# Performance work log

Hardware: AMD Instinct MI355X
Metric: run time of the kernel (lower is better)

## Reference

```python
import jax, jax.numpy as jnp
import numpy as np

B, S, D, H = 2, 2048, 1024, 16
HD = D // H  # 64
MASK_VAL = -10000.0


def setup_inputs() -> dict:
    key = jax.random.key(0)
    ks = jax.random.split(key, 8)
    sc = 0.02
    q_features = jax.random.normal(ks[0], (B, S, D), jnp.float32)
    kv_features = jax.random.normal(ks[1], (B, S, D), jnp.float32)
    # causal mask, broadcastable (1,1,S,S)
    mask = jnp.tril(jnp.ones((S, S), jnp.bool_))[None, None]
    Wq = jax.random.normal(ks[2], (D, D), jnp.float32) * sc
    bq = jnp.zeros((D,), jnp.float32)
    Wkv = jax.random.normal(ks[3], (D, 2 * D), jnp.float32) * sc
    bkv = jnp.zeros((2 * D,), jnp.float32)
    Wp = jax.random.normal(ks[4], (D, D), jnp.float32) * sc
    bp = jnp.zeros((D,), jnp.float32)
    return {"q_features": q_features, "kv_features": kv_features, "mask": mask,
            "Wq": Wq, "bq": bq, "Wkv": Wkv, "bkv": bkv, "Wp": Wp, "bp": bp}


def _split_heads(t):
    # (B,S,D) -> (B,H,S,HD)
    return t.reshape(B, S, H, HD).transpose(0, 2, 1, 3)


def reference(q_features, kv_features, mask, Wq, bq, Wkv, bkv, Wp, bp):
    query = q_features @ Wq + bq            # (B,S,D)
    kv = kv_features @ Wkv + bkv            # (B,S,2D)
    key, value = jnp.split(kv, 2, axis=-1)
    q = _split_heads(query)                 # (B,H,S,HD)
    k = _split_heads(key)
    v = _split_heads(value)
    scores = jnp.einsum('bhqd,bhkd->bhqk', q, k) / jnp.sqrt(jnp.float32(HD))
    scores = jnp.where(mask, scores, jnp.asarray(MASK_VAL, scores.dtype))
    attn = jax.nn.softmax(scores, axis=-1)  # (B,H,S,S)
    out = jnp.einsum('bhqk,bhkd->bhqd', attn, v)
    out = out.transpose(0, 2, 1, 3).reshape(B, S, D)  # merge heads
    return out @ Wp + bp
```

## Files before the change

### kernel.cpp

```cpp
#include <hip/hip_runtime.h>

typedef unsigned short u16;
typedef unsigned int u32;
typedef __attribute__((ext_vector_type(4))) unsigned short us4;
typedef __attribute__((ext_vector_type(8))) unsigned short us8;
typedef __attribute__((ext_vector_type(4))) short s16x4;
typedef __attribute__((ext_vector_type(8))) __bf16 bf16x8;
typedef __attribute__((ext_vector_type(4))) float floatx4;

#define S_ 2048
#define D_ 1024
#define QSC 0.18033688f

__device__ __forceinline__ float b2f(u16 u) {
  unsigned v = ((unsigned)u) << 16;
  return __builtin_bit_cast(float, v);
}
__device__ __forceinline__ u16 f2bf(float f) {
  unsigned u = __builtin_bit_cast(unsigned, f);
  unsigned r = (u + 0x7fffu + ((u >> 16) & 1u)) >> 16;
  return (u16)r;
}
__device__ __forceinline__ u16 f2bf_rhu(float f) {
  return (u16)((__builtin_bit_cast(unsigned, f) + 0x8000u) >> 16);
}

typedef const __attribute__((address_space(1))) u32* gas_t;
typedef __attribute__((address_space(3))) u32* las_t;
__device__ __forceinline__ void gload16(const u16* g, u16* l) {
  __builtin_amdgcn_global_load_lds((gas_t)g, (las_t)l, 16, 0, 0);
}

#define PBAR()                                   \
  {                                              \
    __builtin_amdgcn_sched_barrier(0);           \
    asm volatile("" ::: "memory");               \
    __builtin_amdgcn_s_barrier();                \
    asm volatile("" ::: "memory");               \
    __builtin_amdgcn_sched_barrier(0);           \
  }
#define WAITVM(N) asm volatile("s_waitcnt vmcnt(" #N ")" ::: "memory")

__global__ __launch_bounds__(256) void prep(
    const float* __restrict__ qf, const float* __restrict__ kvf,
    const float* __restrict__ Wq, const float* __restrict__ Wkv,
    const float* __restrict__ Wp, u16* __restrict__ qa, u16* __restrict__ kva,
    u16* __restrict__ Wqt, u16* __restrict__ Wkvt, u16* __restrict__ Wpt) {
  int bid = blockIdx.x, tid = threadIdx.x;
  if (bid < 4096) {
    const float* src = (bid < 2048) ? qf : kvf;
    u16* dst = (bid < 2048) ? qa : kva;
    size_t i = ((size_t)(bid & 2047) * 256 + tid) * 8;
    floatx4 a = *(const floatx4*)(src + i);
    floatx4 b = *(const floatx4*)(src + i + 4);
    us8 r;
#pragma unroll
    for (int j = 0; j < 4; j++) { r[j] = f2bf(a[j]); r[4 + j] = f2bf(b[j]); }
    *(us8*)(dst + i) = r;
  } else {
    int t = bid - 4096;
    const float* src; u16* dst; int R, C;
    if (t < 1024)      { src = Wq;  dst = Wqt;  R = 1024; C = 1024; }
    else if (t < 3072) { t -= 1024; src = Wkv; dst = Wkvt; R = 1024; C = 2048; }
    else               { t -= 3072; src = Wp;  dst = Wpt;  R = 1024; C = 1024; }
    int bx = t % (C >> 5), by = t / (C >> 5);
    __shared__ u16 tile[32][33];
    int tx = tid & 31, ty = tid >> 5;
    int x = bx * 32 + tx;
    for (int i = ty; i < 32; i += 8)
      tile[i][tx] = f2bf(src[(size_t)(by * 32 + i) * C + x]);
    __syncthreads();
    int r = tid >> 3, c4 = tid & 7;
    us4 v;
#pragma unroll
    for (int j = 0; j < 4; j++) v[j] = tile[c4 * 4 + j][r];
    *(us4*)&dst[(size_t)(bx * 32 + r) * R + by * 32 + c4 * 4] = v;
  }
}

template <int TM, int TN, int MODE>
__device__ __forceinline__ void gemm4w(
    const u16* __restrict__ A, const u16* __restrict__ Bt,
    const float* __restrict__ bias, void* __restrict__ C0,
    u16* __restrict__ C1, int N, int m0, int n0, u16* smem, float cscale) {
  constexpr int MF = TM / 32, NF = TN / 32;
  constexpr int ASZ = TM * 64;
  constexpr int SLOT = (TM + TN) * 64;
  int tid = threadIdx.x;
  int w = tid >> 6, lane = tid & 63;
  int quad = lane >> 4, l16 = lane & 15;
  int wr = w >> 1, wc = w & 1;

  int gch = ((lane & 7) ^ ((lane >> 3) & 7)) << 3;
  const u16* Ag = A + (size_t)(m0 + w * (TM / 4) + (lane >> 3)) * 1024 + gch;
  const u16* Bg = Bt + (size_t)(n0 + w * (TN / 4) + (lane >> 3)) * 1024 + gch;
  u16* Adst = smem + w * (TM / 4) * 64;
  u16* Bdst = smem + ASZ + w * (TN / 4) * 64;

  int ab = (wr * (TM / 2) + l16) * 64;
  int bb = ASZ + (wc * (TN / 2) + l16) * 64;
  int xk0 = (quad ^ (l16 & 7)) << 3;
  int xk1 = ((4 + quad) ^ (l16 & 7)) << 3;

  floatx4 acc[MF][NF] = {};

#define STAGE4(tn, s_)                                                  \
  {                                                                     \
    _Pragma("unroll") for (int i = 0; i < MF; i++)                      \
      gload16(Ag + (size_t)(tn) * 64 + (size_t)i * 8192,                \
              Adst + (s_) * SLOT + i * 512);                            \
    _Pragma("unroll") for (int i = 0; i < NF; i++)                      \
      gload16(Bg + (size_t)(tn) * 64 + (size_t)i * 8192,                \
              Bdst + (s_) * SLOT + i * 512);                            \
  }

#define COMPUTE4(SOFF)                                                  \
  {                                                                     \
    _Pragma("unroll") for (int kk = 0; kk < 2; kk++) {                  \
      int xk = kk ? xk1 : xk0;                                          \
      bf16x8 bfr[NF];                                                   \
      _Pragma("unroll") for (int nf = 0; nf < NF; nf++)                 \
        bfr[nf] = __builtin_bit_cast(bf16x8,                            \
            *(const us8*)&smem[(SOFF) + bb + nf * 1024 + xk]);          \
      _Pragma("unroll") for (int mf = 0; mf < MF; mf++) {               \
        bf16x8 afr = __builtin_bit_cast(bf16x8,                         \
            *(const us8*)&smem[(SOFF) + ab + mf * 1024 + xk]);          \
        _Pragma("unroll") for (int nf = 0; nf < NF; nf++)               \
          acc[mf][nf] = __builtin_amdgcn_mfma_f32_16x16x32_bf16(        \
              afr, bfr[nf], acc[mf][nf], 0, 0, 0);                      \
      }                                                                 \
    }                                                                   \
  }

  STAGE4(0, 0);
  WAITVM(0);
  PBAR();
#pragma unroll 1
  for (int t = 0; t < 16; t += 2) {
    STAGE4(t + 1, 1);
    COMPUTE4(0);
    WAITVM(0);
    PBAR();
    if (t + 2 < 16) STAGE4(t + 2, 0);
    COMPUTE4(SLOT);
    WAITVM(0);
    PBAR();
  }

#undef STAGE4
#undef COMPUTE4

#pragma unroll
  for (int mf = 0; mf < MF; mf++) {
#pragma unroll
    for (int nf = 0; nf < NF; nf++) {
      int col = n0 + wc * (TN / 2) + nf * 16 + l16;
      int rowq = m0 + wr * (TM / 2) + mf * 16 + quad * 4;
      float bv = bias[col];
      if (MODE == 0) {
        u16* o = (u16*)C0;
#pragma unroll
        for (int r = 0; r < 4; r++)
          o[(size_t)(rowq + r) * N + col] = f2bf((acc[mf][nf][r] + bv) * cscale);
      } else if (MODE == 1) {
        float* o = (float*)C0;
#pragma unroll
        for (int r = 0; r < 4; r++)
          o[(size_t)(rowq + r) * N + col] = acc[mf][nf][r] + bv;
      } else {
        if (col < 1024) {
          u16* o = (u16*)C0;
#pragma unroll
          for (int r = 0; r < 4; r++)
            o[(size_t)(rowq + r) * 1024 + col] = f2bf(acc[mf][nf][r] + bv);
        } else {
          int vcol = col - 1024;
          int b = rowq >> 11, s0 = rowq & 2047;
          us4 pv;
#pragma unroll
          for (int r = 0; r < 4; r++) pv[r] = f2bf(acc[mf][nf][r] + bv);
          *(us4*)&C1[((size_t)(b * 1024 + vcol)) * (size_t)S_ + s0] = pv;
        }
      }
    }
  }
}

__global__ __launch_bounds__(256, 2) void gemm_qkv(
    const u16* __restrict__ qa, const u16* __restrict__ kva,
    const u16* __restrict__ Wqt, const u16* __restrict__ Wkvt,
    const float* __restrict__ bq, const float* __restrict__ bkv,
    u16* __restrict__ Qb, u16* __restrict__ Kb, u16* __restrict__ Vt) {
  __shared__ __align__(16) u16 smem[32768];
  int bid = blockIdx.x;
  int work = (bid & 7) * 96 + (bid >> 3);
  if (work < 256) {
    gemm4w<128, 128, 0>(qa, Wqt, bq, Qb, nullptr, 1024,
                        (work >> 3) * 128, (work & 7) * 128, smem, QSC);
  } else {
    int lb = work - 256;
    gemm4w<128, 128, 2>(kva, Wkvt, bkv, Kb, Vt, 2048,
                        (lb >> 4) * 128, (lb & 15) * 128, smem, 1.0f);
  }
}

__global__ __launch_bounds__(256, 3) void gemm_out(
    const u16* __restrict__ AO, const u16* __restrict__ Wpt,
    const float* __restrict__ bp, float* __restrict__ out) {
  __shared__ __align__(16) u16 smem[24576];
  int work = (blockIdx.x & 7) * 64 + (blockIdx.x >> 3);
  gemm4w<128, 64, 1>(AO, Wpt, bp, out, nullptr, 1024,
                     (work >> 4) * 128, (work & 15) * 64, smem, 1.0f);
}

__global__ __launch_bounds__(512) void attn_fwd(
    const u16* __restrict__ Q, const u16* __restrict__ Kb,
    const u16* __restrict__ Vt, u16* __restrict__ O,
    u16* __restrict__ Opart, float* __restrict__ ml) {
  __shared__ __align__(16) u16 sm[16384];
  int tid  = threadIdx.x;
  int w    = tid >> 6, lane = tid & 63;
  int quad = lane >> 4, l16 = lane & 15;
  int bh = blockIdx.x, b = bh >> 4, h = bh & 15;
  int y = blockIdx.y;

  static const signed char yt_[24] = {15,15,7,14,14,13,13,6,12,12,11,11,5,
                                      10,10,9,9,4,8,8,3,2,1,0};
  static const signed char yh_[24] = {0,1,-1,0,1,0,1,-1,0,1,0,1,-1,
                                      0,1,0,1,-1,0,1,-1,-1,-1,-1};
  int t = yt_[y], hh = yh_[y];
  bool split = hh >= 0;
  int kb0, kb1;
  if (split) { kb0 = hh ? (t + 1) : 0; kb1 = hh ? (2 * t + 2) : (t + 1); }
  else       { kb0 = 0; kb1 = 2 * t + 2; }
  int n = kb1 - kb0;

  const size_t row0 = (size_t)b * S_;
  const u16* Kg = Kb + row0 * D_ + h * 64;
  const u16* Vg = Vt + ((size_t)b * 1024 + h * 64) * S_;

  int qlo = t * 128 + w * 16;
  int dkb = qlo >> 6;
  int qg  = (qlo & 63) + l16;

  const u16* qp = Q + (row0 + qlo + l16) * D_ + h * 64 + quad * 8;
  bf16x8 aqv[2];
  aqv[0] = __builtin_bit_cast(bf16x8, *(const us8*)(qp));
  aqv[1] = __builtin_bit_cast(bf16x8, *(const us8*)(qp + 32));

  floatx4 o_[4] = {};
  floatx4 l_acc = {};
  const s16x4 ones4 = {0x3F80, 0x3F80, 0x3F80, 0x3F80};

  int srow = tid >> 3, c8 = tid & 7;
  int woff = srow * 64 + ((c8 ^ (srow & 7)) << 3);
  u16* smK = sm;
  u16* smV = sm + 8192;

  const u16* Kp = Kg + (size_t)(kb0 * 64 + srow) * D_ + c8 * 8;
  const u16* Vp = Vg + (size_t)srow * S_ + kb0 * 64 + c8 * 8;
  us8 pk = *(const us8*)Kp, pv = *(const us8*)Vp;
  *(us8*)&smK[woff] = pk;
  *(us8*)&smV[woff] = pv;
  if (n > 1) {
    Kp += (size_t)64 * D_; Vp += 64;
    pk = *(const us8*)Kp; pv = *(const us8*)Vp;
  }
  __syncthreads();

  for (int i = 0; i < n; i++) {
    int cur = i & 1;
    int kb = kb0 + i;
    if (i + 1 < n) {
      int nxt = (cur ^ 1) * 4096;
      *(us8*)&smK[nxt + woff] = pk;
      *(us8*)&smV[nxt + woff] = pv;
      if (i + 2 < n) {
        Kp += (size_t)64 * D_; Vp += 64;
        pk = *(const us8*)Kp; pv = *(const us8*)Vp;
      }
    }
    if (kb <= dkb) {
      const u16* Ksb = smK + cur * 4096;
      const u16* Vsb = smV + cur * 4096;

      floatx4 s[4] = {};
      __builtin_amdgcn_s_setprio(1);
#pragma unroll
      for (int kk = 0; kk < 2; kk++)
#pragma unroll
        for (int nt = 0; nt < 4; nt++) {
          us8 kf = *(const us8*)&Ksb[(nt * 16 + l16) * 64 +
                                     (((kk * 4 + quad) ^ (l16 & 7)) << 3)];
          s[nt] = __builtin_amdgcn_mfma_f32_16x16x32_bf16(
              __builtin_bit_cast(bf16x8, kf), aqv[kk], s[nt], 0, 0, 0);
        }
      __builtin_amdgcn_s_setprio(0);

      if (kb == dkb) {
#pragma unroll
        for (int nt = 0; nt < 4; nt++)
#pragma unroll
          for (int r = 0; r < 4; r++)
            if (nt * 16 + quad * 4 + r > qg) s[nt][r] = -1e5f;
      }

      s16x4 pb[4];
#pragma unroll
      for (int nt = 0; nt < 4; nt++)
#pragma unroll
        for (int r = 0; r < 4; r++)
          pb[nt][r] = (short)f2bf_rhu(__builtin_amdgcn_exp2f(s[nt][r]));

      __builtin_amdgcn_s_setprio(1);
#pragma unroll
      for (int nt = 0; nt < 4; nt++) {
        l_acc = __builtin_amdgcn_mfma_f32_16x16x16bf16_1k(ones4, pb[nt], l_acc, 0, 0, 0);
#pragma unroll
        for (int mt = 0; mt < 4; mt++) {
          int hd = mt * 16 + l16;
          int chunk = nt * 2 + (quad >> 1);
          us4 vf = *(const us4*)&Vsb[hd * 64 + ((chunk ^ (l16 & 7)) << 3) + (quad & 1) * 4];
          o_[mt] = __builtin_amdgcn_mfma_f32_16x16x16bf16_1k(
              __builtin_bit_cast(s16x4, vf), pb[nt], o_[mt], 0, 0, 0);
        }
      }
      __builtin_amdgcn_s_setprio(0);
    }
    __syncthreads();
  }

  if (!split) {
    float rl = __builtin_amdgcn_rcpf(l_acc[0]);
    size_t orow = (row0 + qlo + l16) * D_ + h * 64;
#pragma unroll
    for (int mt = 0; mt < 4; mt++) {
      us4 ov;
#pragma unroll
      for (int r = 0; r < 4; r++) ov[r] = f2bf(o_[mt][r] * rl);
      *(us4*)&O[orow + mt * 16 + quad * 4] = ov;
    }
  } else {
    int part = (t - 8) * 2 + hh;
    u16* op = Opart + ((size_t)(bh * 16 + part)) * 8192;
    int rloc = w * 16 + l16;
#pragma unroll
    for (int mt = 0; mt < 4; mt++) {
      us4 ov;
#pragma unroll
      for (int r = 0; r < 4; r++) ov[r] = f2bf(o_[mt][r]);
      *(us4*)&op[rloc * 64 + mt * 16 + quad * 4] = ov;
    }
    if (quad == 0)
      ml[(size_t)(bh * 16 + part) * 128 + rloc] = l_acc[0];
  }
}

__global__ __launch_bounds__(256) void combine(
    const u16* __restrict__ Opart, const float* __restrict__ ml,
    u16* __restrict__ O) {
  int bh = blockIdx.x, b = bh >> 4, h = bh & 15;
  int t = 8 + blockIdx.y;
  int p0 = bh * 16 + (t - 8) * 2;
  const u16* o1 = Opart + (size_t)p0 * 8192;
  const u16* o2 = o1 + 8192;
  int row = threadIdx.x >> 1, ch = (threadIdx.x & 1) * 32;
  float l1 = ml[(size_t)p0 * 128 + row];
  float l2 = ml[(size_t)(p0 + 1) * 128 + row];
  float inv = __builtin_amdgcn_rcpf(l1 + l2);
  size_t orow = ((size_t)b * S_ + t * 128 + row) * D_ + h * 64 + ch;
#pragma unroll
  for (int v = 0; v < 4; v++) {
    us8 x1 = *(const us8*)&o1[row * 64 + ch + v * 8];
    us8 x2 = *(const us8*)&o2[row * 64 + ch + v * 8];
    us8 out;
#pragma unroll
    for (int j = 0; j < 8; j++)
      out[j] = f2bf((b2f(x1[j]) + b2f(x2[j])) * inv);
    *(us8*)&O[orow + v * 8] = out;
  }
}

extern "C" void kernel_launch(void* const* d_in, const int* in_sizes, int n_in,
                              void* d_out, int out_size, void* d_ws, size_t ws_size,
                              hipStream_t stream) {
  const float* qf  = (const float*)d_in[0];
  const float* kvf = (const float*)d_in[1];
  const float* Wq  = (const float*)d_in[3];
  const float* bq  = (const float*)d_in[4];
  const float* Wkv = (const float*)d_in[5];
  const float* bkv = (const float*)d_in[6];
  const float* Wp  = (const float*)d_in[7];
  const float* bp  = (const float*)d_in[8];

  char* ws = (char*)d_ws;
  const size_t MB = 1048576;
  u16*   kva  = (u16*)(ws);
  u16*   AO   = (u16*)(ws);
  u16*   Kbp  = (u16*)(ws + 8 * MB);
  u16*   Vtp  = (u16*)(ws + 16 * MB);
  u16*   Wqt  = (u16*)(ws + 24 * MB);
  float* mlp  = (float*)(ws + 24 * MB);
  u16*   Wkvt = (u16*)(ws + 26 * MB);
  u16*   Wpt  = (u16*)(ws + 30 * MB);
  u16*   qa    = (u16*)d_out;
  u16*   Opart = (u16*)d_out;
  u16*   Qb    = (u16*)d_out + (size_t)4 * 1048576;

  prep<<<8192, 256, 0, stream>>>(qf, kvf, Wq, Wkv, Wp, qa, kva, Wqt, Wkvt, Wpt);
  gemm_qkv<<<768, 256, 0, stream>>>(qa, kva, Wqt, Wkvt, bq, bkv, Qb, Kbp, Vtp);
  attn_fwd<<<dim3(32, 24), 512, 0, stream>>>(Qb, Kbp, Vtp, AO, Opart, mlp);
  combine<<<dim3(32, 8), 256, 0, stream>>>(Opart, mlp, AO);
  gemm_out<<<512, 256, 0, stream>>>(AO, Wpt, bp, (float*)d_out);
}
```

Before: 204.2 us.

## Replace QKV GEMM with 256x256-tile, 8-wave, 4-stage pipelined kernel

Adds a gemm256 device routine that computes 256x256 output tiles with 8 waves (2x4), K-step 32, and a 4-slot LDS ring buffer with 3 loads in flight. The QKV projection launch drops from 768 blocks of 256 threads to 192 blocks of 512 threads. The aim is higher arithmetic intensity per LDS/global load and deeper latency hiding. In exchange it needs 128KB of LDS and 128 accumulator floats per thread, so occupancy is lower, and with only 192 blocks the grid may not fill all CUs evenly.

```diff
diff --git a/kernel.cpp b/kernel.cpp
--- a/kernel.cpp
+++ b/kernel.cpp
@@ -78,6 +78,119 @@
   }
 }
 
+template <int MODE>
+__device__ __forceinline__ void gemm256(
+    const u16* __restrict__ A, const u16* __restrict__ Bt,
+    const float* __restrict__ bias, void* __restrict__ C0,
+    u16* __restrict__ C1, int N, int m0, int n0, u16* smem, float cscale) {
+  int tid = threadIdx.x;
+  int w = tid >> 6, lane = tid & 63;
+  int quad = lane >> 4, l16 = lane & 15;
+  int wr = w >> 2, wc = w & 3;
+
+  int srow = w * 32 + (lane >> 2);
+  int gchunk = ((lane & 3) ^ ((lane >> 3) & 3)) << 3;
+  const u16* Asrc = A + (size_t)(m0 + srow) * 1024 + gchunk;
+  const u16* Bsrc = Bt + (size_t)(n0 + srow) * 1024 + gchunk;
+  u16* Adst = smem + w * 1024;
+  u16* Bdst = smem + 32768 + w * 1024;
+
+  int swz = (quad ^ ((l16 >> 1) & 3)) << 3;
+  int aoff = (wr * 128 + l16) * 32 + swz;
+  int boff = 32768 + (wc * 64 + l16) * 32 + swz;
+
+  floatx4 acc[8][4] = {};
+
+#define STG(t)                                                 \
+  {                                                            \
+    int s_ = (t) & 3;                                          \
+    gload16(Asrc + (t) * 32, Adst + s_ * 8192);                \
+    gload16(Asrc + (t) * 32 + 16384, Adst + s_ * 8192 + 512);  \
+    gload16(Bsrc + (t) * 32, Bdst + s_ * 8192);                \
+    gload16(Bsrc + (t) * 32 + 16384, Bdst + s_ * 8192 + 512);  \
+  }
+
+  STG(0); STG(1); STG(2);
+  WAITVM(8);
+  PBAR();
+
+#pragma unroll 1
+  for (int t = 0; t < 32; t++) {
+    int so = (t & 3) * 8192;
+    bf16x8 af[8], bf[4];
+#pragma unroll
+    for (int mf = 0; mf < 8; mf++)
+      af[mf] = __builtin_bit_cast(bf16x8,
+          *(const us8*)&smem[so + aoff + mf * 512]);
+#pragma unroll
+    for (int nf = 0; nf < 4; nf++)
+      bf[nf] = __builtin_bit_cast(bf16x8,
+          *(const us8*)&smem[so + boff + nf * 512]);
+    if (t < 29) STG(t + 3);
+    __builtin_amdgcn_s_setprio(1);
+#pragma unroll
+    for (int mf = 0; mf < 8; mf++)
+#pragma unroll
+      for (int nf = 0; nf < 4; nf++)
+        acc[mf][nf] = __builtin_amdgcn_mfma_f32_16x16x32_bf16(
+            af[mf], bf[nf], acc[mf][nf], 0, 0, 0);
+    __builtin_amdgcn_s_setprio(0);
+    if (t < 29)      { WAITVM(8); }
+    else if (t == 29){ WAITVM(4); }
+    else if (t == 30){ WAITVM(0); }
+    if (t < 31) PBAR();
+  }
+#undef STG
+
+#pragma unroll
+  for (int mf = 0; mf < 8; mf++) {
+#pragma unroll
+    for (int nf = 0; nf < 4; nf++) {
+      int col = n0 + wc * 64 + nf * 16 + l16;
+      int rowq = m0 + wr * 128 + mf * 16 + quad * 4;
+      float bv = bias[col];
+      if (MODE == 0) {
+        u16* o = (u16*)C0;
+#pragma unroll
+        for (int r = 0; r < 4; r++)
+          o[(size_t)(rowq + r) * N + col] = f2bf((acc[mf][nf][r] + bv) * cscale);
+      } else {
+        if (col < 1024) {
+          u16* o = (u16*)C0;
+#pragma unroll
+          for (int r = 0; r < 4; r++)
+            o[(size_t)(rowq + r) * 1024 + col] = f2bf(acc[mf][nf][r] + bv);
+        } else {
+          int vcol = col - 1024;
+          int b = rowq >> 11, s0 = rowq & 2047;
+          us4 pv;
+#pragma unroll
+          for (int r = 0; r < 4; r++) pv[r] = f2bf(acc[mf][nf][r] + bv);
+          *(us4*)&C1[((size_t)(b * 1024 + vcol)) * (size_t)S_ + s0] = pv;
+        }
+      }
+    }
+  }
+}
+
+__global__ __launch_bounds__(512, 2) void gemm_qkv(
+    const u16* __restrict__ qa, const u16* __restrict__ kva,
+    const u16* __restrict__ Wqt, const u16* __restrict__ Wkvt,
+    const float* __restrict__ bq, const float* __restrict__ bkv,
+    u16* __restrict__ Qb, u16* __restrict__ Kb, u16* __restrict__ Vt) {
+  __shared__ __align__(16) u16 smem[65536];
+  int bid = blockIdx.x;
+  int work = (bid & 7) * 24 + (bid >> 3);
+  if (work < 64) {
+    gemm256<0>(qa, Wqt, bq, Qb, nullptr, 1024,
+               (work >> 2) * 256, (work & 3) * 256, smem, QSC);
+  } else {
+    int lb = work - 64;
+    gemm256<2>(kva, Wkvt, bkv, Kb, Vt, 2048,
+               (lb >> 3) * 256, (lb & 7) * 256, smem, 1.0f);
+  }
+}
+
 template <int TM, int TN, int MODE>
 __device__ __forceinline__ void gemm4w(
     const u16* __restrict__ A, const u16* __restrict__ Bt,
@@ -186,24 +299,6 @@
   }
 }
 
-__global__ __launch_bounds__(256, 2) void gemm_qkv(
-    const u16* __restrict__ qa, const u16* __restrict__ kva,
-    const u16* __restrict__ Wqt, const u16* __restrict__ Wkvt,
-    const float* __restrict__ bq, const float* __restrict__ bkv,
-    u16* __restrict__ Qb, u16* __restrict__ Kb, u16* __restrict__ Vt) {
-  __shared__ __align__(16) u16 smem[32768];
-  int bid = blockIdx.x;
-  int work = (bid & 7) * 96 + (bid >> 3);
-  if (work < 256) {
-    gemm4w<128, 128, 0>(qa, Wqt, bq, Qb, nullptr, 1024,
-                        (work >> 3) * 128, (work & 7) * 128, smem, QSC);
-  } else {
-    int lb = work - 256;
-    gemm4w<128, 128, 2>(kva, Wkvt, bkv, Kb, Vt, 2048,
-                        (lb >> 4) * 128, (lb & 15) * 128, smem, 1.0f);
-  }
-}
-
 __global__ __launch_bounds__(256, 3) void gemm_out(
     const u16* __restrict__ AO, const u16* __restrict__ Wpt,
     const float* __restrict__ bp, float* __restrict__ out) {
@@ -408,7 +503,7 @@
   u16*   Qb    = (u16*)d_out + (size_t)4 * 1048576;
 
   prep<<<8192, 256, 0, stream>>>(qf, kvf, Wq, Wkv, Wp, qa, kva, Wqt, Wkvt, Wpt);
-  gemm_qkv<<<768, 256, 0, stream>>>(qa, kva, Wqt, Wkvt, bq, bkv, Qb, Kbp, Vtp);
+  gemm_qkv<<<192, 512, 0, stream>>>(qa, kva, Wqt, Wkvt, bq, bkv, Qb, Kbp, Vtp);
   attn_fwd<<<dim3(32, 24), 512, 0, stream>>>(Qb, Kbp, Vtp, AO, Opart, mlp);
   combine<<<dim3(32, 8), 256, 0, stream>>>(Opart, mlp, AO);
   gemm_out<<<512, 256, 0, stream>>>(AO, Wpt, bp, (float*)d_out);
```

Measured after the change: 207.3 us. Within noise of the previous version (+1.5%).
